# Optimization experiments

Measured on AMD Instinct MI355X. Metric: run time of the kernel, lower is better.

The kernel has to match this reference:

```python
import jax, jax.numpy as jnp
import numpy as np

B, H, HKV, S, D = 2, 16, 4, 4096, 64
BN = 64            # block size (BLOCK_N)
G = 64             # num_global_tokens (== one block)
NB = S // BN       # total kv blocks
WINDOW = 3         # local window blocks per query block
NRAND = 3          # random blocks per query block
BPQ = WINDOW + NRAND
SCALE = 1.0 / float(np.sqrt(D))
NEG = -1e30


def setup_inputs() -> dict:
    key = jax.random.key(0)
    kq, kk, kv = jax.random.split(key, 3)
    q = jax.random.normal(kq, (B, H, S, D), jnp.float32)
    k = jax.random.normal(kk, (B, HKV, S, D), jnp.float32)
    v = jax.random.normal(kv, (B, HKV, S, D), jnp.float32)
    # 4 contiguous segments per batch row
    seg = jnp.arange(S, dtype=jnp.int32) // (S // 4)
    segment_ids = jnp.broadcast_to(seg, (B, S))
    alibi_slopes = jnp.asarray(2.0 ** (-8.0 * np.arange(1, H + 1) / H), jnp.float32)
    # block indices: per query block, window blocks + random blocks; -1 = skip
    rng = np.random.default_rng(0)
    bi = np.full((NB, BPQ), -1, np.int64)
    first = G // BN  # first sparse query block (global block handled separately)
    for i in range(first, NB):
        win = [b if first <= b < NB else -1 for b in (i - 1, i, i + 1)]
        rnd = rng.integers(first, NB, size=NRAND).tolist()
        bi[i] = win + rnd
    block_indices = jnp.asarray(bi)
    return {"q": q, "k": k, "v": v, "segment_ids": segment_ids,
            "block_indices": block_indices, "alibi_slopes": alibi_slopes}


def _softmax_attend(scores, values):
    m = jnp.max(scores, axis=-1, keepdims=True)
    p = jnp.exp(scores - m)
    l = jnp.sum(p, axis=-1, keepdims=True)
    l = jnp.where(l == 0.0, 1.0, l)
    return jnp.einsum('...qk,...kd->...qd', p / l, values)


def _forward(q, k, v, alibi_slopes, segment_ids, block_indices):
    hpg = H // HKV
    kf = jnp.repeat(k, hpg, axis=1)  # [B,H,S,D]
    vf = jnp.repeat(v, hpg, axis=1)
    pos = jnp.arange(S, dtype=jnp.float32)
    seg = segment_ids

    # ---- global queries: first G tokens attend to the full sequence ----
    qg = q[:, :, :G]
    sc_g = jnp.einsum('bhgd,bhsd->bhgs', qg, kf) * SCALE
    bias_g = -alibi_slopes[None, :, None, None] * jnp.abs(
        pos[:G][None, None, :, None] - pos[None, None, None, :])
    sc_g = sc_g + bias_g
    same_g = (seg[:, :G, None] == seg[:, None, :]) & (seg[:, :G, None] >= 0)
    sc_g = jnp.where(same_g[:, None], sc_g, NEG)
    out_g = _softmax_attend(sc_g, vf)  # [B,H,G,D]

    # ---- sparse query blocks: global KV + gathered window/random blocks ----
    first = G // BN
    nq = NB - first
    K = BPQ * BN
    qs = q[:, :, G:].reshape(B, H, nq, BN, D)
    bi = block_indices[first:]                      # [nq,BPQ]
    bi_safe = jnp.where(bi >= 0, bi, 0)
    kb = kf.reshape(B, H, NB, BN, D)[:, :, bi_safe].reshape(B, H, nq, K, D)
    vb = vf.reshape(B, H, NB, BN, D)[:, :, bi_safe].reshape(B, H, nq, K, D)
    kposi = (bi_safe * BN)[:, :, None] + jnp.arange(BN)      # [nq,BPQ,BN]
    valid = (jnp.broadcast_to((bi >= 0)[:, :, None], kposi.shape)
             & (kposi < S) & (kposi >= G)).reshape(nq, K)
    kposi = kposi.reshape(nq, K)
    kposf = kposi.astype(jnp.float32)
    qpos = jnp.arange(G, S, dtype=jnp.float32).reshape(nq, BN)
    qseg = seg[:, G:].reshape(B, nq, BN)
    kseg = seg[:, kposi]                            # [B,nq,K]

    sc_b = jnp.einsum('bhqmd,bhqnd->bhqmn', qs, kb) * SCALE
    sc_b = sc_b - alibi_slopes[None, :, None, None, None] * jnp.abs(
        qpos[:, :, None] - kposf[:, None, :])[None, None]
    same_b = (qseg[:, :, :, None] == kseg[:, :, None, :]) & (qseg[:, :, :, None] >= 0)
    sc_b = jnp.where((same_b & valid[None, :, None, :])[:, None], sc_b, NEG)

    gk, gv = kf[:, :, :G], vf[:, :, :G]
    sc_gk = jnp.einsum('bhqmd,bhgd->bhqmg', qs, gk) * SCALE
    sc_gk = sc_gk - alibi_slopes[None, :, None, None, None] * jnp.abs(
        qpos[:, :, None] - pos[:G][None, None, :])[None, None]
    gseg = seg[:, :G]
    same_gk = (qseg[:, :, :, None] == gseg[:, None, None, :]) & (qseg[:, :, :, None] >= 0)
    sc_gk = jnp.where(same_gk[:, None], sc_gk, NEG)

    scores = jnp.concatenate([sc_gk, sc_b], axis=-1)         # [B,H,nq,BN,G+K]
    vals = jnp.concatenate(
        [jnp.broadcast_to(gv[:, :, None], (B, H, nq, G, D)), vb], axis=-2)
    out_s = _softmax_attend(scores, vals).reshape(B, H, S - G, D)

    return jnp.concatenate([out_g, out_s], axis=2)           # [B,H,S,D]


def reference(q, k, v, segment_ids, block_indices, alibi_slopes):
    return _forward(q, k, v, alibi_slopes, segment_ids, block_indices)
```

## Files before the change

### kernel.cpp

```cpp
#include <hip/hip_runtime.h>
#include <hip/hip_bf16.h>

#define B_ 2
#define H_ 16
#define HKV_ 4
#define S_ 4096
#define D_ 64
#define BN_ 64
#define NB_ 64
#define BPQ_ 6
#define QSCALE_LOG2 0.18033688f
#define LOG2E 1.44269504f
#define LDK 72
#define NSPLIT0 4
#define PART_ 4224

typedef short bf16x8 __attribute__((ext_vector_type(8)));
typedef short bf16x4v __attribute__((ext_vector_type(4)));
typedef float f32x4 __attribute__((ext_vector_type(4)));
typedef unsigned int u32x4 __attribute__((ext_vector_type(4)));

static __device__ __forceinline__ short f2bf(float f) {
    unsigned u = __builtin_bit_cast(unsigned, f);
    unsigned r = u + 0x7FFFu + ((u >> 16) & 1u);
    return (short)(r >> 16);
}

static __device__ __forceinline__ unsigned cvt_pk_bf16(float lo, float hi) {
    unsigned r;
    asm("v_cvt_pk_bf16_f32 %0, %1, %2" : "=v"(r) : "v"(lo), "v"(hi));
    return r;
}

__global__ __launch_bounds__(256) void sparse_attn_main(
    const float* __restrict__ q,
    const float* __restrict__ k,
    const float* __restrict__ v,
    const int* __restrict__ seg,
    const int* __restrict__ bidx,
    const float* __restrict__ slopes,
    float* __restrict__ out,
    float* __restrict__ ws)
{
    __shared__ short kc[BN_][LDK];
    __shared__ short vt[D_][LDK];
    __shared__ int vlist[17];
    __shared__ int vcount;

    const int qbx  = blockIdx.x;
    int qb, split;
    if (qbx < NB_) { qb = qbx; split = 0; }
    else           { qb = 0;   split = qbx - (NB_ - 1); }
    const bool split_path = (qb == 0);

    const int bh   = blockIdx.y;
    const int b    = bh / H_;
    const int h    = bh % H_;
    const int hkv  = h / (H_ / HKV_);
    const int tid  = threadIdx.x;
    const int wave = tid >> 6;
    const int lane = tid & 63;
    const int l16  = lane & 15;
    const int lhi  = lane >> 4;

    const float slope2 = slopes[h] * LOG2E;
    const int   qseg   = seg[b * S_ + qb * BN_];

    if (wave == 0) {
        const int n = split_path ? 16 : (1 + BPQ_);
        int cand = -1;
        if (lane < n) {
            if (split_path)       cand = split + 4 * lane;
            else if (lane == 0)   cand = 0;
            else                  cand = bidx[qb * BPQ_ + lane - 1];
        }
        bool ok = false;
        if (cand >= 0) {
            int ks_ = seg[b * S_ + cand * BN_];
            ok = (qseg >= 0) && (ks_ == qseg);
        }
        unsigned long long m = __ballot(ok);
        if (ok) {
            int rank = __popcll(m & ((1ull << lane) - 1ull));
            vlist[rank] = cand;
        }
        if (lane == 0) vcount = (int)__popcll(m);
    }

    const int qrow = qb * BN_ + wave * 16 + l16;
    const float qpos = (float)qrow;
    const float* qp = q + (((size_t)(b * H_ + h)) * S_ + qrow) * D_;
    bf16x8 qf[2];
#pragma unroll
    for (int kk = 0; kk < 2; ++kk)
#pragma unroll
        for (int i = 0; i < 8; ++i)
            qf[kk][i] = f2bf(qp[kk * 32 + lhi * 8 + i] * QSCALE_LOG2);

    f32x4 oacc[4] = {};
    float mrun = -1e30f, lrun = 0.f;

    const float* kb_ptr = k + ((size_t)(b * HKV_ + hkv)) * S_ * D_;
    const float* vb_ptr = v + ((size_t)(b * HKV_ + hkv)) * S_ * D_;

    __syncthreads();
    const int nval = vcount;

    float4 kr0, kr1, kr2, kr3, vr0, vr1, vr2, vr3;
#define ISSUE_LOADS(CBLK) do { \
        const float4* ks_ = (const float4*)(kb_ptr + (size_t)(CBLK) * (BN_ * D_)); \
        const float4* vs_ = (const float4*)(vb_ptr + (size_t)(CBLK) * (BN_ * D_)); \
        kr0 = ks_[tid];       kr1 = ks_[tid + 256]; \
        kr2 = ks_[tid + 512]; kr3 = ks_[tid + 768]; \
        vr0 = vs_[tid];       vr1 = vs_[tid + 256]; \
        vr2 = vs_[tid + 512]; vr3 = vs_[tid + 768]; \
    } while (0)

#define WRITE_STAGE(IT, KR, VR) do { \
        int idx_ = tid + (IT) * 256; \
        int key_ = idx_ >> 4; \
        int d0_  = (idx_ & 15) * 4; \
        bf16x4v k4_ = { f2bf(KR.x), f2bf(KR.y), f2bf(KR.z), f2bf(KR.w) }; \
        *(bf16x4v*)&kc[key_][d0_] = k4_; \
        int sw_ = key_ ^ (((d0_ >> 2) & 7) << 3); \
        vt[d0_ + 0][sw_] = f2bf(VR.x); \
        vt[d0_ + 1][sw_] = f2bf(VR.y); \
        vt[d0_ + 2][sw_] = f2bf(VR.z); \
        vt[d0_ + 3][sw_] = f2bf(VR.w); \
    } while (0)

    if (nval > 0) ISSUE_LOADS(vlist[0]);

    for (int i = 0; i < nval; ++i) {
        const int kbase = vlist[i] * BN_;

        __syncthreads();
        WRITE_STAGE(0, kr0, vr0);
        WRITE_STAGE(1, kr1, vr1);
        WRITE_STAGE(2, kr2, vr2);
        WRITE_STAGE(3, kr3, vr3);
        if (i + 1 < nval) ISSUE_LOADS(vlist[i + 1]);
        __syncthreads();

        f32x4 sacc[4];
#pragma unroll
        for (int nt = 0; nt < 4; ++nt) {
            f32x4 s = {};
#pragma unroll
            for (int kk = 0; kk < 2; ++kk) {
                bf16x8 kf_ = *(const bf16x8*)&kc[nt * 16 + l16][kk * 32 + lhi * 8];
                s = __builtin_amdgcn_mfma_f32_16x16x32_bf16(kf_, qf[kk], s, 0, 0, 0);
            }
            sacc[nt] = s;
        }

        float p_[4][4];
        float mx = -1e30f;
#pragma unroll
        for (int nt = 0; nt < 4; ++nt)
#pragma unroll
            for (int r = 0; r < 4; ++r) {
                float kpos = (float)(kbase + nt * 16 + lhi * 4 + r);
                float sc = sacc[nt][r] - slope2 * fabsf(qpos - kpos);
                p_[nt][r] = sc;
                mx = fmaxf(mx, sc);
            }
        mx = fmaxf(mx, __shfl_xor(mx, 16));
        mx = fmaxf(mx, __shfl_xor(mx, 32));
        const float mn = fmaxf(mrun, mx);
        float sum = 0.f;
#pragma unroll
        for (int nt = 0; nt < 4; ++nt)
#pragma unroll
            for (int r = 0; r < 4; ++r) {
                float p = exp2f(p_[nt][r] - mn);
                p_[nt][r] = p;
                sum += p;
            }
        sum += __shfl_xor(sum, 16);
        sum += __shfl_xor(sum, 32);
        const float corr = exp2f(mrun - mn);
        mrun = mn;
        lrun = lrun * corr + sum;
#pragma unroll
        for (int dt = 0; dt < 4; ++dt) oacc[dt] *= corr;

        unsigned pk_[4][2];
#pragma unroll
        for (int nt = 0; nt < 4; ++nt) {
            pk_[nt][0] = cvt_pk_bf16(p_[nt][0], p_[nt][1]);
            pk_[nt][1] = cvt_pk_bf16(p_[nt][2], p_[nt][3]);
        }

#pragma unroll
        for (int kk = 0; kk < 2; ++kk) {
            u32x4 pw = { pk_[2 * kk][0], pk_[2 * kk][1],
                         pk_[2 * kk + 1][0], pk_[2 * kk + 1][1] };
            bf16x8 pf = __builtin_bit_cast(bf16x8, pw);
#pragma unroll
            for (int dt = 0; dt < 4; ++dt) {
                const short* vrow = &vt[dt * 16 + l16][0];
                const int sv8 = ((4 * dt + (l16 >> 2)) & 7) << 3;
                bf16x4v lo = *(const bf16x4v*)&vrow[(kk * 32 + 4 * lhi) ^ sv8];
                bf16x4v hi = *(const bf16x4v*)&vrow[(kk * 32 + 16 + 4 * lhi) ^ sv8];
                bf16x8 vf = __builtin_shufflevector(lo, hi, 0, 1, 2, 3, 4, 5, 6, 7);
                oacc[dt] = __builtin_amdgcn_mfma_f32_16x16x32_bf16(vf, pf, oacc[dt], 0, 0, 0);
            }
        }
    }

    if (split_path) {
        float* wsp = ws + (size_t)(bh * NSPLIT0 + split) * PART_;
        const int m = wave * 16 + l16;
#pragma unroll
        for (int dt = 0; dt < 4; ++dt) {
            float4 o4 = { oacc[dt][0], oacc[dt][1], oacc[dt][2], oacc[dt][3] };
            *(float4*)&wsp[m * D_ + dt * 16 + 4 * lhi] = o4;
        }
        if (lhi == 0) {
            wsp[4096 + m] = mrun;
            wsp[4160 + m] = lrun;
        }
    } else {
        const float inv = 1.0f / (lrun == 0.f ? 1.f : lrun);
        float* op = out + ((size_t)bh * S_ + qrow) * D_;
#pragma unroll
        for (int dt = 0; dt < 4; ++dt) {
            float4 o4 = { oacc[dt][0] * inv, oacc[dt][1] * inv,
                          oacc[dt][2] * inv, oacc[dt][3] * inv };
            *(float4*)&op[dt * 16 + 4 * lhi] = o4;
        }
    }
}

__global__ __launch_bounds__(256) void sparse_attn_combine(
    const float* __restrict__ ws,
    float* __restrict__ out)
{
    const int bh  = blockIdx.x;
    const int t   = threadIdx.x;
    const int row = t >> 2;
    const int d0  = (t & 3) * 16;

    const float* base = ws + (size_t)bh * NSPLIT0 * PART_;
    float ms[NSPLIT0], ls[NSPLIT0];
    float M = -1e30f;
#pragma unroll
    for (int s = 0; s < NSPLIT0; ++s) {
        ms[s] = base[s * PART_ + 4096 + row];
        ls[s] = base[s * PART_ + 4160 + row];
        M = fmaxf(M, ms[s]);
    }
    float w[NSPLIT0];
    float L = 0.f;
#pragma unroll
    for (int s = 0; s < NSPLIT0; ++s) {
        w[s] = exp2f(ms[s] - M);
        L += w[s] * ls[s];
    }
    const float inv = 1.0f / (L == 0.f ? 1.f : L);

    float* op = out + ((size_t)bh * S_ + row) * D_ + d0;
#pragma unroll
    for (int j = 0; j < 16; ++j) {
        float acc = 0.f;
#pragma unroll
        for (int s = 0; s < NSPLIT0; ++s)
            acc += w[s] * base[s * PART_ + row * D_ + d0 + j];
        op[j] = acc * inv;
    }
}

extern "C" void kernel_launch(void* const* d_in, const int* in_sizes, int n_in,
                              void* d_out, int out_size, void* d_ws, size_t ws_size,
                              hipStream_t stream) {
    const float* q      = (const float*)d_in[0];
    const float* k      = (const float*)d_in[1];
    const float* v      = (const float*)d_in[2];
    const int*   seg    = (const int*)d_in[3];
    const int*   bidx   = (const int*)d_in[4];
    const float* slopes = (const float*)d_in[5];
    float*       out    = (float*)d_out;
    float*       ws     = (float*)d_ws;

    dim3 grid(NB_ + (NSPLIT0 - 1), B_ * H_);
    sparse_attn_main<<<grid, 256, 0, stream>>>(q, k, v, seg, bidx, slopes, out, ws);
    sparse_attn_combine<<<dim3(B_ * H_), 256, 0, stream>>>(ws, out);
}
```

Measured before the change: 139.5 us.

## Split KV blocks across two wave groups per workgroup and merge softmax states

Doubles the workgroup to 512 threads so two groups of four waves each process alternating KV blocks for the same query block, each with its own LDS staging buffers. The two partial online-softmax states are merged through shared memory at the end. This halves the serial per-block loop length and raises latency hiding. It also switches K conversion to packed bf16 conversion and folds the ALiBi distance computation into an fma. The cost is doubled LDS use, an extra merge step with barriers, and idle waves when the valid block count is odd.

```diff
diff --git a/kernel.cpp b/kernel.cpp
--- a/kernel.cpp
+++ b/kernel.cpp
@@ -32,7 +32,7 @@
     return r;
 }
 
-__global__ __launch_bounds__(256) void sparse_attn_main(
+__global__ __launch_bounds__(512) void sparse_attn_main(
     const float* __restrict__ q,
     const float* __restrict__ k,
     const float* __restrict__ v,
@@ -42,8 +42,7 @@
     float* __restrict__ out,
     float* __restrict__ ws)
 {
-    __shared__ short kc[BN_][LDK];
-    __shared__ short vt[D_][LDK];
+    __shared__ __align__(16) char smem[36864];
     __shared__ int vlist[17];
     __shared__ int vcount;
 
@@ -59,9 +58,15 @@
     const int hkv  = h / (H_ / HKV_);
     const int tid  = threadIdx.x;
     const int wave = tid >> 6;
+    const int strm = wave >> 2;
+    const int w4   = wave & 3;
     const int lane = tid & 63;
     const int l16  = lane & 15;
     const int lhi  = lane >> 4;
+    const int tis  = tid & 255;
+
+    short* kcp = (short*)smem + strm * 4608;
+    short* vtp = (short*)(smem + 18432) + strm * 4608;
 
     const float slope2 = slopes[h] * LOG2E;
     const int   qseg   = seg[b * S_ + qb * BN_];
@@ -87,7 +92,7 @@
         if (lane == 0) vcount = (int)__popcll(m);
     }
 
-    const int qrow = qb * BN_ + wave * 16 + l16;
+    const int qrow = qb * BN_ + w4 * 16 + l16;
     const float qpos = (float)qrow;
     const float* qp = q + (((size_t)(b * H_ + h)) * S_ + qrow) * D_;
     bf16x8 qf[2];
@@ -105,42 +110,50 @@
 
     __syncthreads();
     const int nval = vcount;
+    const int nr   = (nval + 1) >> 1;
 
     float4 kr0, kr1, kr2, kr3, vr0, vr1, vr2, vr3;
 #define ISSUE_LOADS(CBLK) do { \
         const float4* ks_ = (const float4*)(kb_ptr + (size_t)(CBLK) * (BN_ * D_)); \
         const float4* vs_ = (const float4*)(vb_ptr + (size_t)(CBLK) * (BN_ * D_)); \
-        kr0 = ks_[tid];       kr1 = ks_[tid + 256]; \
-        kr2 = ks_[tid + 512]; kr3 = ks_[tid + 768]; \
-        vr0 = vs_[tid];       vr1 = vs_[tid + 256]; \
-        vr2 = vs_[tid + 512]; vr3 = vs_[tid + 768]; \
+        kr0 = ks_[tis];       kr1 = ks_[tis + 256]; \
+        kr2 = ks_[tis + 512]; kr3 = ks_[tis + 768]; \
+        vr0 = vs_[tis];       vr1 = vs_[tis + 256]; \
+        vr2 = vs_[tis + 512]; vr3 = vs_[tis + 768]; \
     } while (0)
 
 #define WRITE_STAGE(IT, KR, VR) do { \
-        int idx_ = tid + (IT) * 256; \
+        int idx_ = tis + (IT) * 256; \
         int key_ = idx_ >> 4; \
         int d0_  = (idx_ & 15) * 4; \
-        bf16x4v k4_ = { f2bf(KR.x), f2bf(KR.y), f2bf(KR.z), f2bf(KR.w) }; \
-        *(bf16x4v*)&kc[key_][d0_] = k4_; \
+        unsigned p0_ = cvt_pk_bf16(KR.x, KR.y); \
+        unsigned p1_ = cvt_pk_bf16(KR.z, KR.w); \
+        uint2 kp_ = { p0_, p1_ }; \
+        *(uint2*)&kcp[key_ * LDK + d0_] = kp_; \
         int sw_ = key_ ^ (((d0_ >> 2) & 7) << 3); \
-        vt[d0_ + 0][sw_] = f2bf(VR.x); \
-        vt[d0_ + 1][sw_] = f2bf(VR.y); \
-        vt[d0_ + 2][sw_] = f2bf(VR.z); \
-        vt[d0_ + 3][sw_] = f2bf(VR.w); \
+        vtp[(d0_ + 0) * LDK + sw_] = f2bf(VR.x); \
+        vtp[(d0_ + 1) * LDK + sw_] = f2bf(VR.y); \
+        vtp[(d0_ + 2) * LDK + sw_] = f2bf(VR.z); \
+        vtp[(d0_ + 3) * LDK + sw_] = f2bf(VR.w); \
     } while (0)
 
-    if (nval > 0) ISSUE_LOADS(vlist[0]);
-
-    for (int i = 0; i < nval; ++i) {
-        const int kbase = vlist[i] * BN_;
+    if (strm < nval) ISSUE_LOADS(vlist[strm]);
+
+    for (int r = 0; r < nr; ++r) {
+        const int c = 2 * r + strm;
+        const bool have = (c < nval);
+        const int kbase = have ? vlist[c] * BN_ : 0;
 
         __syncthreads();
-        WRITE_STAGE(0, kr0, vr0);
-        WRITE_STAGE(1, kr1, vr1);
-        WRITE_STAGE(2, kr2, vr2);
-        WRITE_STAGE(3, kr3, vr3);
-        if (i + 1 < nval) ISSUE_LOADS(vlist[i + 1]);
+        if (have) {
+            WRITE_STAGE(0, kr0, vr0);
+            WRITE_STAGE(1, kr1, vr1);
+            WRITE_STAGE(2, kr2, vr2);
+            WRITE_STAGE(3, kr3, vr3);
+            if (c + 2 < nval) ISSUE_LOADS(vlist[c + 2]);
+        }
         __syncthreads();
+        if (!have) continue;
 
         f32x4 sacc[4];
 #pragma unroll
@@ -148,21 +161,21 @@
             f32x4 s = {};
 #pragma unroll
             for (int kk = 0; kk < 2; ++kk) {
-                bf16x8 kf_ = *(const bf16x8*)&kc[nt * 16 + l16][kk * 32 + lhi * 8];
+                bf16x8 kf_ = *(const bf16x8*)&kcp[(nt * 16 + l16) * LDK + kk * 32 + lhi * 8];
                 s = __builtin_amdgcn_mfma_f32_16x16x32_bf16(kf_, qf[kk], s, 0, 0, 0);
             }
             sacc[nt] = s;
         }
 
+        const float dbase = qpos - (float)(kbase + lhi * 4);
         float p_[4][4];
         float mx = -1e30f;
 #pragma unroll
         for (int nt = 0; nt < 4; ++nt)
 #pragma unroll
-            for (int r = 0; r < 4; ++r) {
-                float kpos = (float)(kbase + nt * 16 + lhi * 4 + r);
-                float sc = sacc[nt][r] - slope2 * fabsf(qpos - kpos);
-                p_[nt][r] = sc;
+            for (int r2 = 0; r2 < 4; ++r2) {
+                float sc = fmaf(-slope2, fabsf(dbase - (float)(nt * 16 + r2)), sacc[nt][r2]);
+                p_[nt][r2] = sc;
                 mx = fmaxf(mx, sc);
             }
         mx = fmaxf(mx, __shfl_xor(mx, 16));
@@ -172,9 +185,9 @@
 #pragma unroll
         for (int nt = 0; nt < 4; ++nt)
 #pragma unroll
-            for (int r = 0; r < 4; ++r) {
-                float p = exp2f(p_[nt][r] - mn);
-                p_[nt][r] = p;
+            for (int r2 = 0; r2 < 4; ++r2) {
+                float p = exp2f(p_[nt][r2] - mn);
+                p_[nt][r2] = p;
                 sum += p;
             }
         sum += __shfl_xor(sum, 16);
@@ -199,7 +212,7 @@
             bf16x8 pf = __builtin_bit_cast(bf16x8, pw);
 #pragma unroll
             for (int dt = 0; dt < 4; ++dt) {
-                const short* vrow = &vt[dt * 16 + l16][0];
+                const short* vrow = &vtp[(dt * 16 + l16) * LDK];
                 const int sv8 = ((4 * dt + (l16 >> 2)) & 7) << 3;
                 bf16x4v lo = *(const bf16x4v*)&vrow[(kk * 32 + 4 * lhi) ^ sv8];
                 bf16x4v hi = *(const bf16x4v*)&vrow[(kk * 32 + 16 + 4 * lhi) ^ sv8];
@@ -209,20 +222,52 @@
         }
     }
 
+    float* obuf = (float*)smem;
+    float* ml   = (float*)(smem + 18432);
+    __syncthreads();
+    if (strm == 1) {
+        float* orow = obuf + (w4 * 16 + l16) * 68;
+#pragma unroll
+        for (int dt = 0; dt < 4; ++dt) {
+            float4 o4 = { oacc[dt][0], oacc[dt][1], oacc[dt][2], oacc[dt][3] };
+            *(float4*)&orow[dt * 16 + 4 * lhi] = o4;
+        }
+        if (lhi == 0) {
+            ml[w4 * 16 + l16]      = mrun;
+            ml[64 + w4 * 16 + l16] = lrun;
+        }
+    }
+    __syncthreads();
+    if (strm != 0) return;
+
+    const float m1 = ml[w4 * 16 + l16];
+    const float l1 = ml[64 + w4 * 16 + l16];
+    const float mM = fmaxf(mrun, m1);
+    const float w0 = exp2f(mrun - mM);
+    const float w1 = exp2f(m1 - mM);
+    const float lM = w0 * lrun + w1 * l1;
+    const float* orow = obuf + (w4 * 16 + l16) * 68;
+#pragma unroll
+    for (int dt = 0; dt < 4; ++dt) {
+        float4 o4 = *(const float4*)&orow[dt * 16 + 4 * lhi];
+        f32x4 o1 = { o4.x, o4.y, o4.z, o4.w };
+        oacc[dt] = oacc[dt] * w0 + o1 * w1;
+    }
+
     if (split_path) {
         float* wsp = ws + (size_t)(bh * NSPLIT0 + split) * PART_;
-        const int m = wave * 16 + l16;
+        const int m = w4 * 16 + l16;
 #pragma unroll
         for (int dt = 0; dt < 4; ++dt) {
             float4 o4 = { oacc[dt][0], oacc[dt][1], oacc[dt][2], oacc[dt][3] };
             *(float4*)&wsp[m * D_ + dt * 16 + 4 * lhi] = o4;
         }
         if (lhi == 0) {
-            wsp[4096 + m] = mrun;
-            wsp[4160 + m] = lrun;
+            wsp[4096 + m] = mM;
+            wsp[4160 + m] = lM;
         }
     } else {
-        const float inv = 1.0f / (lrun == 0.f ? 1.f : lrun);
+        const float inv = 1.0f / (lM == 0.f ? 1.f : lM);
         float* op = out + ((size_t)bh * S_ + qrow) * D_;
 #pragma unroll
         for (int dt = 0; dt < 4; ++dt) {
@@ -284,6 +329,6 @@
     float*       ws     = (float*)d_ws;
 
     dim3 grid(NB_ + (NSPLIT0 - 1), B_ * H_);
-    sparse_attn_main<<<grid, 256, 0, stream>>>(q, k, v, seg, bidx, slopes, out, ws);
+    sparse_attn_main<<<grid, 512, 0, stream>>>(q, k, v, seg, bidx, slopes, out, ws);
     sparse_attn_combine<<<dim3(B_ * H_), 256, 0, stream>>>(ws, out);
 }
```

Result: slower. 143.8 us (+3.1%).

## Share KV tiles across the four GQA heads per block with double-buffered LDS

Applied to the files above, without the earlier changes.

Each workgroup now handles all four query heads of one KV head (512 threads, two waves per head, each wave covering 32 query rows), so every K/V block is loaded and converted to bf16 once instead of four times. Shared memory is double-buffered so the next block is staged while the current one is computed, with one barrier per iteration instead of two. The split-K workspace layout and the combine kernel are re-indexed to per-KV-head groups. This cuts global K/V traffic and conversion work but raises register pressure per wave and quarters the number of workgroups, which may hurt occupancy and load balance.

```diff
diff --git a/kernel.cpp b/kernel.cpp
--- a/kernel.cpp
+++ b/kernel.cpp
@@ -4,6 +4,7 @@
 #define B_ 2
 #define H_ 16
 #define HKV_ 4
+#define HPG_ 4
 #define S_ 4096
 #define D_ 64
 #define BN_ 64
@@ -13,7 +14,7 @@
 #define LOG2E 1.44269504f
 #define LDK 72
 #define NSPLIT0 4
-#define PART_ 4224
+#define PART2_ 16896
 
 typedef short bf16x8 __attribute__((ext_vector_type(8)));
 typedef short bf16x4v __attribute__((ext_vector_type(4)));
@@ -32,7 +33,7 @@
     return r;
 }
 
-__global__ __launch_bounds__(256) void sparse_attn_main(
+__global__ __launch_bounds__(512, 4) void sparse_attn_main(
     const float* __restrict__ q,
     const float* __restrict__ k,
     const float* __restrict__ v,
@@ -42,8 +43,8 @@
     float* __restrict__ out,
     float* __restrict__ ws)
 {
-    __shared__ short kc[BN_][LDK];
-    __shared__ short vt[D_][LDK];
+    __shared__ __align__(16) short kc[2][BN_ * LDK];
+    __shared__ __align__(16) short vt[2][BN_ * LDK];
     __shared__ int vlist[17];
     __shared__ int vcount;
 
@@ -53,15 +54,17 @@
     else           { qb = 0;   split = qbx - (NB_ - 1); }
     const bool split_path = (qb == 0);
 
-    const int bh   = blockIdx.y;
-    const int b    = bh / H_;
-    const int h    = bh % H_;
-    const int hkv  = h / (H_ / HKV_);
+    const int y    = blockIdx.y;
+    const int b    = y / HKV_;
+    const int hkv  = y % HKV_;
     const int tid  = threadIdx.x;
     const int wave = tid >> 6;
+    const int g    = wave >> 1;
+    const int half = wave & 1;
     const int lane = tid & 63;
     const int l16  = lane & 15;
     const int lhi  = lane >> 4;
+    const int h    = hkv * HPG_ + g;
 
     const float slope2 = slopes[h] * LOG2E;
     const int   qseg   = seg[b * S_ + qb * BN_];
@@ -75,7 +78,7 @@
             else                  cand = bidx[qb * BPQ_ + lane - 1];
         }
         bool ok = false;
-        if (cand >= 0) {
+        if (cand >= 0 && cand < NB_) {
             int ks_ = seg[b * S_ + cand * BN_];
             ok = (qseg >= 0) && (ks_ == qseg);
         }
@@ -87,148 +90,159 @@
         if (lane == 0) vcount = (int)__popcll(m);
     }
 
-    const int qrow = qb * BN_ + wave * 16 + l16;
-    const float qpos = (float)qrow;
-    const float* qp = q + (((size_t)(b * H_ + h)) * S_ + qrow) * D_;
-    bf16x8 qf[2];
-#pragma unroll
-    for (int kk = 0; kk < 2; ++kk)
-#pragma unroll
-        for (int i = 0; i < 8; ++i)
-            qf[kk][i] = f2bf(qp[kk * 32 + lhi * 8 + i] * QSCALE_LOG2);
-
-    f32x4 oacc[4] = {};
-    float mrun = -1e30f, lrun = 0.f;
+    bf16x8 qf[2][2];
+    float qpos[2];
+#pragma unroll
+    for (int j = 0; j < 2; ++j) {
+        const int qrow = qb * BN_ + half * 32 + j * 16 + l16;
+        qpos[j] = (float)qrow;
+        const float* qp = q + (((size_t)(b * H_ + h)) * S_ + qrow) * D_;
+#pragma unroll
+        for (int kk = 0; kk < 2; ++kk)
+#pragma unroll
+            for (int i = 0; i < 8; ++i)
+                qf[j][kk][i] = f2bf(qp[kk * 32 + lhi * 8 + i] * QSCALE_LOG2);
+    }
+
+    f32x4 oacc[2][4] = {};
+    float mrun[2] = { -1e30f, -1e30f }, lrun[2] = { 0.f, 0.f };
 
     const float* kb_ptr = k + ((size_t)(b * HKV_ + hkv)) * S_ * D_;
     const float* vb_ptr = v + ((size_t)(b * HKV_ + hkv)) * S_ * D_;
 
-    __syncthreads();
-    const int nval = vcount;
-
-    float4 kr0, kr1, kr2, kr3, vr0, vr1, vr2, vr3;
+    float4 kr0, kr1, vr0, vr1;
 #define ISSUE_LOADS(CBLK) do { \
         const float4* ks_ = (const float4*)(kb_ptr + (size_t)(CBLK) * (BN_ * D_)); \
         const float4* vs_ = (const float4*)(vb_ptr + (size_t)(CBLK) * (BN_ * D_)); \
-        kr0 = ks_[tid];       kr1 = ks_[tid + 256]; \
-        kr2 = ks_[tid + 512]; kr3 = ks_[tid + 768]; \
-        vr0 = vs_[tid];       vr1 = vs_[tid + 256]; \
-        vr2 = vs_[tid + 512]; vr3 = vs_[tid + 768]; \
+        kr0 = ks_[tid];       kr1 = ks_[tid + 512]; \
+        vr0 = vs_[tid];       vr1 = vs_[tid + 512]; \
     } while (0)
 
-#define WRITE_STAGE(IT, KR, VR) do { \
-        int idx_ = tid + (IT) * 256; \
-        int key_ = idx_ >> 4; \
-        int d0_  = (idx_ & 15) * 4; \
-        bf16x4v k4_ = { f2bf(KR.x), f2bf(KR.y), f2bf(KR.z), f2bf(KR.w) }; \
-        *(bf16x4v*)&kc[key_][d0_] = k4_; \
+#define WST1(P, IDX, KR, VR) do { \
+        int key_ = (IDX) >> 4; \
+        int d0_  = ((IDX) & 15) * 4; \
+        uint2 kp_ = { cvt_pk_bf16(KR.x, KR.y), cvt_pk_bf16(KR.z, KR.w) }; \
+        *(uint2*)&kc[P][key_ * LDK + d0_] = kp_; \
         int sw_ = key_ ^ (((d0_ >> 2) & 7) << 3); \
-        vt[d0_ + 0][sw_] = f2bf(VR.x); \
-        vt[d0_ + 1][sw_] = f2bf(VR.y); \
-        vt[d0_ + 2][sw_] = f2bf(VR.z); \
-        vt[d0_ + 3][sw_] = f2bf(VR.w); \
+        vt[P][(d0_ + 0) * LDK + sw_] = f2bf(VR.x); \
+        vt[P][(d0_ + 1) * LDK + sw_] = f2bf(VR.y); \
+        vt[P][(d0_ + 2) * LDK + sw_] = f2bf(VR.z); \
+        vt[P][(d0_ + 3) * LDK + sw_] = f2bf(VR.w); \
     } while (0)
-
-    if (nval > 0) ISSUE_LOADS(vlist[0]);
-
-    for (int i = 0; i < nval; ++i) {
-        const int kbase = vlist[i] * BN_;
-
-        __syncthreads();
-        WRITE_STAGE(0, kr0, vr0);
-        WRITE_STAGE(1, kr1, vr1);
-        WRITE_STAGE(2, kr2, vr2);
-        WRITE_STAGE(3, kr3, vr3);
-        if (i + 1 < nval) ISSUE_LOADS(vlist[i + 1]);
-        __syncthreads();
-
-        f32x4 sacc[4];
-#pragma unroll
-        for (int nt = 0; nt < 4; ++nt) {
-            f32x4 s = {};
+#define WRITE_STAGE(P) do { WST1(P, tid, kr0, vr0); WST1(P, tid + 512, kr1, vr1); } while (0)
+
+    __syncthreads();
+    const int nval = vcount;
+
+    ISSUE_LOADS(vlist[0]);
+    WRITE_STAGE(0);
+    if (nval > 1) ISSUE_LOADS(vlist[1]);
+    __syncthreads();
+
+    for (int c = 0; c < nval; ++c) {
+        const int p = c & 1;
+        const int kbase = vlist[c] * BN_;
+
+        if (c + 1 < nval) {
+            WRITE_STAGE(p ^ 1);
+            if (c + 2 < nval) ISSUE_LOADS(vlist[c + 2]);
+        }
+
+        f32x4 sacc[2][4] = {};
+#pragma unroll
+        for (int nt = 0; nt < 4; ++nt)
 #pragma unroll
             for (int kk = 0; kk < 2; ++kk) {
-                bf16x8 kf_ = *(const bf16x8*)&kc[nt * 16 + l16][kk * 32 + lhi * 8];
-                s = __builtin_amdgcn_mfma_f32_16x16x32_bf16(kf_, qf[kk], s, 0, 0, 0);
-            }
-            sacc[nt] = s;
-        }
-
-        float p_[4][4];
-        float mx = -1e30f;
-#pragma unroll
-        for (int nt = 0; nt < 4; ++nt)
-#pragma unroll
-            for (int r = 0; r < 4; ++r) {
-                float kpos = (float)(kbase + nt * 16 + lhi * 4 + r);
-                float sc = sacc[nt][r] - slope2 * fabsf(qpos - kpos);
-                p_[nt][r] = sc;
-                mx = fmaxf(mx, sc);
-            }
-        mx = fmaxf(mx, __shfl_xor(mx, 16));
-        mx = fmaxf(mx, __shfl_xor(mx, 32));
-        const float mn = fmaxf(mrun, mx);
-        float sum = 0.f;
-#pragma unroll
-        for (int nt = 0; nt < 4; ++nt)
-#pragma unroll
-            for (int r = 0; r < 4; ++r) {
-                float p = exp2f(p_[nt][r] - mn);
-                p_[nt][r] = p;
-                sum += p;
-            }
-        sum += __shfl_xor(sum, 16);
-        sum += __shfl_xor(sum, 32);
-        const float corr = exp2f(mrun - mn);
-        mrun = mn;
-        lrun = lrun * corr + sum;
-#pragma unroll
-        for (int dt = 0; dt < 4; ++dt) oacc[dt] *= corr;
-
-        unsigned pk_[4][2];
-#pragma unroll
-        for (int nt = 0; nt < 4; ++nt) {
-            pk_[nt][0] = cvt_pk_bf16(p_[nt][0], p_[nt][1]);
-            pk_[nt][1] = cvt_pk_bf16(p_[nt][2], p_[nt][3]);
+                bf16x8 kf_ = *(const bf16x8*)&kc[p][(nt * 16 + l16) * LDK + kk * 32 + lhi * 8];
+                sacc[0][nt] = __builtin_amdgcn_mfma_f32_16x16x32_bf16(kf_, qf[0][kk], sacc[0][nt], 0, 0, 0);
+                sacc[1][nt] = __builtin_amdgcn_mfma_f32_16x16x32_bf16(kf_, qf[1][kk], sacc[1][nt], 0, 0, 0);
+            }
+
+#pragma unroll
+        for (int j = 0; j < 2; ++j) {
+            const float dbase = qpos[j] - (float)(kbase + lhi * 4);
+            float mx = -1e30f;
+#pragma unroll
+            for (int nt = 0; nt < 4; ++nt)
+#pragma unroll
+                for (int r2 = 0; r2 < 4; ++r2) {
+                    float sc = fmaf(-slope2, fabsf(dbase - (float)(nt * 16 + r2)), sacc[j][nt][r2]);
+                    sacc[j][nt][r2] = sc;
+                    mx = fmaxf(mx, sc);
+                }
+            mx = fmaxf(mx, __shfl_xor(mx, 16));
+            mx = fmaxf(mx, __shfl_xor(mx, 32));
+            const float mn = fmaxf(mrun[j], mx);
+            float sum = 0.f;
+#pragma unroll
+            for (int nt = 0; nt < 4; ++nt)
+#pragma unroll
+                for (int r2 = 0; r2 < 4; ++r2) {
+                    float pe = exp2f(sacc[j][nt][r2] - mn);
+                    sacc[j][nt][r2] = pe;
+                    sum += pe;
+                }
+            sum += __shfl_xor(sum, 16);
+            sum += __shfl_xor(sum, 32);
+            const float corr = exp2f(mrun[j] - mn);
+            mrun[j] = mn;
+            lrun[j] = lrun[j] * corr + sum;
+#pragma unroll
+            for (int dt = 0; dt < 4; ++dt) oacc[j][dt] *= corr;
         }
 
 #pragma unroll
         for (int kk = 0; kk < 2; ++kk) {
-            u32x4 pw = { pk_[2 * kk][0], pk_[2 * kk][1],
-                         pk_[2 * kk + 1][0], pk_[2 * kk + 1][1] };
-            bf16x8 pf = __builtin_bit_cast(bf16x8, pw);
+            bf16x8 pf[2];
+#pragma unroll
+            for (int j = 0; j < 2; ++j) {
+                u32x4 pw = { cvt_pk_bf16(sacc[j][2 * kk][0],     sacc[j][2 * kk][1]),
+                             cvt_pk_bf16(sacc[j][2 * kk][2],     sacc[j][2 * kk][3]),
+                             cvt_pk_bf16(sacc[j][2 * kk + 1][0], sacc[j][2 * kk + 1][1]),
+                             cvt_pk_bf16(sacc[j][2 * kk + 1][2], sacc[j][2 * kk + 1][3]) };
+                pf[j] = __builtin_bit_cast(bf16x8, pw);
+            }
 #pragma unroll
             for (int dt = 0; dt < 4; ++dt) {
-                const short* vrow = &vt[dt * 16 + l16][0];
+                const short* vrow = &vt[p][(dt * 16 + l16) * LDK];
                 const int sv8 = ((4 * dt + (l16 >> 2)) & 7) << 3;
                 bf16x4v lo = *(const bf16x4v*)&vrow[(kk * 32 + 4 * lhi) ^ sv8];
                 bf16x4v hi = *(const bf16x4v*)&vrow[(kk * 32 + 16 + 4 * lhi) ^ sv8];
                 bf16x8 vf = __builtin_shufflevector(lo, hi, 0, 1, 2, 3, 4, 5, 6, 7);
-                oacc[dt] = __builtin_amdgcn_mfma_f32_16x16x32_bf16(vf, pf, oacc[dt], 0, 0, 0);
-            }
-        }
+                oacc[0][dt] = __builtin_amdgcn_mfma_f32_16x16x32_bf16(vf, pf[0], oacc[0][dt], 0, 0, 0);
+                oacc[1][dt] = __builtin_amdgcn_mfma_f32_16x16x32_bf16(vf, pf[1], oacc[1][dt], 0, 0, 0);
+            }
+        }
+
+        __syncthreads();
     }
 
     if (split_path) {
-        float* wsp = ws + (size_t)(bh * NSPLIT0 + split) * PART_;
-        const int m = wave * 16 + l16;
-#pragma unroll
-        for (int dt = 0; dt < 4; ++dt) {
-            float4 o4 = { oacc[dt][0], oacc[dt][1], oacc[dt][2], oacc[dt][3] };
-            *(float4*)&wsp[m * D_ + dt * 16 + 4 * lhi] = o4;
-        }
-        if (lhi == 0) {
-            wsp[4096 + m] = mrun;
-            wsp[4160 + m] = lrun;
+        float* wsp = ws + (size_t)((b * HKV_ + hkv) * NSPLIT0 + split) * PART2_;
+#pragma unroll
+        for (int j = 0; j < 2; ++j) {
+            const int row = half * 32 + j * 16 + l16;
+#pragma unroll
+            for (int dt = 0; dt < 4; ++dt) {
+                float4 o4 = { oacc[j][dt][0], oacc[j][dt][1], oacc[j][dt][2], oacc[j][dt][3] };
+                *(float4*)&wsp[g * 4096 + row * 64 + dt * 16 + 4 * lhi] = o4;
+            }
+            if (lhi == 0) {
+                wsp[16384 + g * 64 + row] = mrun[j];
+                wsp[16640 + g * 64 + row] = lrun[j];
+            }
         }
     } else {
-        const float inv = 1.0f / (lrun == 0.f ? 1.f : lrun);
-        float* op = out + ((size_t)bh * S_ + qrow) * D_;
-#pragma unroll
-        for (int dt = 0; dt < 4; ++dt) {
-            float4 o4 = { oacc[dt][0] * inv, oacc[dt][1] * inv,
-                          oacc[dt][2] * inv, oacc[dt][3] * inv };
-            *(float4*)&op[dt * 16 + 4 * lhi] = o4;
+#pragma unroll
+        for (int j = 0; j < 2; ++j) {
+            const float inv = 1.0f / (lrun[j] == 0.f ? 1.f : lrun[j]);
+            float* op = out + (((size_t)(b * H_ + h)) * S_ + qb * BN_ + half * 32 + j * 16 + l16) * D_;
+#pragma unroll
+            for (int dt = 0; dt < 4; ++dt) {
+                float4 o4 = { oacc[j][dt][0] * inv, oacc[j][dt][1] * inv,
+                              oacc[j][dt][2] * inv, oacc[j][dt][3] * inv };
+                *(float4*)&op[dt * 16 + 4 * lhi] = o4;
+            }
         }
     }
 }
@@ -238,17 +252,21 @@
     float* __restrict__ out)
 {
     const int bh  = blockIdx.x;
+    const int b   = bh / H_;
+    const int h   = bh % H_;
+    const int hkv = h >> 2;
+    const int g   = h & 3;
     const int t   = threadIdx.x;
     const int row = t >> 2;
     const int d0  = (t & 3) * 16;
 
-    const float* base = ws + (size_t)bh * NSPLIT0 * PART_;
+    const float* base = ws + (size_t)(b * HKV_ + hkv) * NSPLIT0 * PART2_;
     float ms[NSPLIT0], ls[NSPLIT0];
     float M = -1e30f;
 #pragma unroll
     for (int s = 0; s < NSPLIT0; ++s) {
-        ms[s] = base[s * PART_ + 4096 + row];
-        ls[s] = base[s * PART_ + 4160 + row];
+        ms[s] = base[s * PART2_ + 16384 + g * 64 + row];
+        ls[s] = base[s * PART2_ + 16640 + g * 64 + row];
         M = fmaxf(M, ms[s]);
     }
     float w[NSPLIT0];
@@ -262,12 +280,12 @@
 
     float* op = out + ((size_t)bh * S_ + row) * D_ + d0;
 #pragma unroll
-    for (int j = 0; j < 16; ++j) {
+    for (int jj = 0; jj < 16; ++jj) {
         float acc = 0.f;
 #pragma unroll
         for (int s = 0; s < NSPLIT0; ++s)
-            acc += w[s] * base[s * PART_ + row * D_ + d0 + j];
-        op[j] = acc * inv;
+            acc += w[s] * base[s * PART2_ + g * 4096 + row * 64 + d0 + jj];
+        op[jj] = acc * inv;
     }
 }
 
@@ -283,7 +301,7 @@
     float*       out    = (float*)d_out;
     float*       ws     = (float*)d_ws;
 
-    dim3 grid(NB_ + (NSPLIT0 - 1), B_ * H_);
-    sparse_attn_main<<<grid, 256, 0, stream>>>(q, k, v, seg, bidx, slopes, out, ws);
+    dim3 grid(NB_ + (NSPLIT0 - 1), B_ * HKV_);
+    sparse_attn_main<<<grid, 512, 0, stream>>>(q, k, v, seg, bidx, slopes, out, ws);
     sparse_attn_combine<<<dim3(B_ * H_), 256, 0, stream>>>(ws, out);
 }
```

Measured after the change: 161.6 us. +15.9%, slower.
